# Kernel optimization log

Measured on AMD Instinct MI355X. Metric: run time of the kernel, lower is better.

## Reference

```python
import math
import jax, jax.numpy as jnp
import numpy as np

D = 2048
N = 16
B = 2
L = 4096
SCALE = math.sqrt(1.0 / float(N))


def setup_inputs() -> dict:
    key = jax.random.key(0)
    ks = jax.random.split(key, 6)
    x = jax.random.normal(ks[0], (B, D, L), dtype=jnp.float32)
    alpha = 0.2 * jax.random.normal(ks[1], (D, N, 1), dtype=jnp.float32)
    delta = 0.2 * jax.random.normal(ks[2], (D, N, 1), dtype=jnp.float32)
    theta = 0.2 * jax.random.normal(ks[3], (D, 1, 1), dtype=jnp.float32)
    gamma = jax.random.normal(ks[4], (D, N, 2), dtype=jnp.float32)
    omega = jax.random.normal(ks[5], (D,), dtype=jnp.float32)
    return {"x": x, "alpha": alpha, "delta": delta, "theta": theta,
            "gamma": gamma, "omega": omega}


def _coeffs(alpha, delta, theta, gamma):
    p = jax.nn.sigmoid(alpha)                       # (D, N, 1)
    d = jax.nn.sigmoid(delta)                       # (D, N, 1)
    wave = jnp.arange(1, N + 1, dtype=jnp.float32).reshape(1, N, 1)
    base = jax.nn.sigmoid(theta) * (2.0 * math.pi / float(N))  # (D,1,1)
    phi = wave * base                               # (D, N, 1)
    q = (1.0 - p * d).astype(jnp.complex64) * jnp.exp(1j * phi)  # (D, N, 1)
    gam = (gamma[..., 0] + 1j * gamma[..., 1]) * SCALE            # (D, N)
    return p, q, gam


def _fftconv_real(x, k):
    # x: (B, D, L), k: (D, L)  -> causal conv, keep first L samples
    n = L + L - 1
    n_fft = 1 << (n - 1).bit_length()
    X = jnp.fft.rfft(x, n=n_fft)                    # (B, D, n_fft//2+1)
    K = jnp.fft.rfft(k, n=n_fft)[None]              # (1, D, n_fft//2+1)
    y = jnp.fft.irfft(X * K, n=n_fft)[..., :L]
    return y.astype(x.dtype)


def reference(x, alpha, delta, theta, gamma, omega):
    p, q, gam = _coeffs(alpha, delta, theta, gamma)
    # kernel_d[t] = Re( sum_n p_dn * gamma_dn * q_dn^t )
    t = jnp.arange(L, dtype=jnp.float32)
    V = jnp.exp(t[None, None, :] * jnp.log(q))      # (D, N, L) = q^t
    kernel = jnp.real(jnp.sum(p * gam[..., None] * V, axis=1))  # (D, L)
    y = _fftconv_real(x, kernel) + x * omega[None, :, None]
    # last state: h_t = q * h_{t-1} + p * x_t  (hx = None)
    qs = q[..., 0]                                   # (D, N)
    ps = p[..., 0]                                   # (D, N)
    xs = jnp.moveaxis(x, -1, 0)                      # (L, B, D)
    h0 = jnp.zeros((B, D, N), dtype=jnp.complex64)

    def step(h, xt):
        # xt: (B, D); px_t = p_dn * x_t[b,d]
        h = qs[None] * h + ps[None] * xt[..., None].astype(jnp.complex64)
        return h, None

    h_last, _ = jax.lax.scan(step, h0, xs)
    h_ri = jnp.stack([h_last.real, h_last.imag], axis=-1)  # (B, D, N, 2)
    return y, h_ri
```

## Files before the change

kernel.cpp:

```cpp
#include <hip/hip_runtime.h>
#include <math.h>


constexpr int kD = 2048, kN = 16, kB = 2, kL = 4096;
constexpr int kT   = 128;
constexpr int kCH  = kL / kT;
constexpr int kRPB = 4;
constexpr int kGrid = (kB * kD) / kRPB;
constexpr float kSCALE = 0.25f;

__global__ __launch_bounds__(kT, 2) void fused_kernel(
    const float* __restrict__ x,     const float* __restrict__ alpha,
    const float* __restrict__ delta, const float* __restrict__ theta,
    const float* __restrict__ gamma, const float* __restrict__ omega,
    float* __restrict__ y,           float* __restrict__ hout)
{
    __shared__ float c2a[2][kN], ccc[2][kN], caa[2][kN], cbb[2][kN];
    __shared__ float cc1[2][kN], cc2[2][kN], cpr[2][kN];
    __shared__ float pubs[2][kN], pubp[2][kN];

    const int tid   = threadIdx.x;
    const int llane = tid & 63;
    const bool w1   = (tid >= 64);
    const int row0  = blockIdx.x * kRPB;

    float4 tb[8];
    {
        const float4* xp = (const float4*)(x + (size_t)row0 * kL + (size_t)tid * kCH);
#pragma unroll
        for (int k = 0; k < 8; k++) tb[k] = xp[k];
    }

#pragma unroll 1
    for (int r = 0; r < kRPB; ++r) {
        const int row = row0 + r;
        const int d   = row & (kD - 1);
        const int pp  = r & 1;

        if (tid < kN) {
            int n = tid, i = d * kN + n;
            float p  = 1.0f / (1.0f + expf(-alpha[i]));
            float dd = 1.0f / (1.0f + expf(-delta[i]));
            float th = 1.0f / (1.0f + expf(-theta[d]));
            float phi = (float)(n + 1) * th * 0.39269908169872414f;
            float rr = 1.0f - p * dd;
            float sn, cs;
            sincosf(phi, &sn, &cs);
            float a = rr * cs, b = rr * sn;
            float gr = p * kSCALE * gamma[2 * i];
            float gi = -(p * kSCALE * gamma[2 * i + 1]);
            c2a[pp][n] = a + a;
            ccc[pp][n] = __builtin_fmaf(a, a, b * b);
            caa[pp][n] = a;
            cbb[pp][n] = b;
            cc1[pp][n] = gr;
            cc2[pp][n] = __builtin_fmaf(gi, b, -(gr * a));
            cpr[pp][n] = p;
        }

        float xs[kCH];
#pragma unroll
        for (int k = 0; k < 8; k++) {
            xs[4*k+0] = tb[k].x; xs[4*k+1] = tb[k].y;
            xs[4*k+2] = tb[k].z; xs[4*k+3] = tb[k].w;
        }
        __syncthreads();

        float twoa[kN], cc[kN];
#pragma unroll
        for (int n = 0; n < kN; n++) { twoa[n] = c2a[pp][n]; cc[n] = ccc[pp][n]; }

        float ss[kN], sq[kN];
#pragma unroll
        for (int n = 0; n < kN; n++) { ss[n] = xs[0]; sq[n] = 0.0f; }
#pragma unroll
        for (int j = 1; j < kCH; j++) {
            float xj = xs[j];
#pragma unroll
            for (int n = 0; n < kN; n++) {
                float t  = __builtin_fmaf(-cc[n], sq[n], xj);
                float sn = __builtin_fmaf(twoa[n], ss[n], t);
                sq[n] = ss[n];
                ss[n] = sn;
            }
        }

        float al[kN], be[kN];
        {
            float aa[kN];
#pragma unroll
            for (int n = 0; n < kN; n++) {
                aa[n] = caa[pp][n];
                al[n] = twoa[n];
                be[n] = 1.0f;
            }
#pragma unroll
            for (int sdb = 0; sdb < 4; sdb++) {
#pragma unroll
                for (int n = 0; n < kN; n++) {
                    float t  = __builtin_fmaf(-cc[n], be[n], aa[n] * al[n]);
                    float nb = __builtin_fmaf(-cc[n], be[n] * be[n], al[n] * al[n]);
                    al[n] = (al[n] + al[n]) * t;
                    be[n] = nb;
                }
            }
        }

        float Wa[kN], Wb[kN];
#pragma unroll
        for (int n = 0; n < kN; n++) { Wa[n] = al[n]; Wb[n] = be[n]; }
#pragma unroll
        for (int rd = 0; rd < 6; rd++) {
            const int sh = 1 << rd;
#pragma unroll
            for (int n = 0; n < kN; n++) {
                float cb  = cc[n] * be[n];
                float e00 = __builtin_fmaf(twoa[n], al[n], -cb);
                float e01 = -(cc[n] * al[n]);
                float ts  = __shfl_up(ss[n], (unsigned)sh, 64);
                float tp  = __shfl_up(sq[n], (unsigned)sh, 64);
                if (llane >= sh) {
                    ss[n] = __builtin_fmaf(e00, ts,
                            __builtin_fmaf(e01, tp, ss[n]));
                    sq[n] = __builtin_fmaf(al[n], ts,
                            __builtin_fmaf(-cb, tp, sq[n]));
                }
            }
            if (w1 && (llane & sh)) {
#pragma unroll
                for (int n = 0; n < kN; n++) {
                    float t1 = Wa[n] * al[n];
                    float t2 = Wb[n] * be[n];
                    float t3 = __builtin_fmaf(Wa[n], be[n], al[n] * Wb[n]);
                    Wa[n] = __builtin_fmaf(twoa[n], t1, -(cc[n] * t3));
                    Wb[n] = __builtin_fmaf(-cc[n], t2, t1);
                }
            }
            if (rd < 5) {
#pragma unroll
                for (int n = 0; n < kN; n++) {
                    float t  = __builtin_fmaf(-cc[n], be[n],
                               0.5f * (twoa[n] * al[n]));
                    float nb = __builtin_fmaf(-cc[n], be[n] * be[n],
                                              al[n] * al[n]);
                    al[n] = (al[n] + al[n]) * t;
                    be[n] = nb;
                }
            }
        }

        if (tid == 63) {
#pragma unroll
            for (int n = 0; n < kN; n++) { pubs[pp][n] = ss[n]; pubp[pp][n] = sq[n]; }
        }
        __syncthreads();
        if (w1) {
#pragma unroll
            for (int n = 0; n < kN; n++) {
                float cb  = cc[n] * Wb[n];
                float e00 = __builtin_fmaf(twoa[n], Wa[n], -cb);
                float e01 = -(cc[n] * Wa[n]);
                float ps  = pubs[pp][n], pq = pubp[pp][n];
                ss[n] = __builtin_fmaf(e00, ps,
                        __builtin_fmaf(e01, pq, ss[n]));
                sq[n] = __builtin_fmaf(Wa[n], ps,
                        __builtin_fmaf(-cb, pq, sq[n]));
            }
        }

        if (tid == kT - 1) {
            float4* hp = (float4*)(hout + (size_t)row * (kN * 2));
#pragma unroll
            for (int k = 0; k < kN / 2; k++) {
                int n0 = 2 * k, n1 = 2 * k + 1;
                float hr0 = cpr[pp][n0] *
                            __builtin_fmaf(-caa[pp][n0], sq[n0], ss[n0]);
                float hi0 = cpr[pp][n0] * cbb[pp][n0] * sq[n0];
                float hr1 = cpr[pp][n1] *
                            __builtin_fmaf(-caa[pp][n1], sq[n1], ss[n1]);
                float hi1 = cpr[pp][n1] * cbb[pp][n1] * sq[n1];
                hp[k] = make_float4(hr0, hi0, hr1, hi1);
            }
        }

#pragma unroll
        for (int n = 0; n < kN; n++) {
            float ts = __shfl_up(ss[n], 1, 64);
            float tp = __shfl_up(sq[n], 1, 64);
            ss[n] = ts; sq[n] = tp;
        }
        if (llane == 0) {
#pragma unroll
            for (int n = 0; n < kN; n++) {
                ss[n] = (tid == 0) ? 0.0f : pubs[pp][n];
                sq[n] = (tid == 0) ? 0.0f : pubp[pp][n];
            }
        }

        if (r + 1 < kRPB) {
            const float4* xn = (const float4*)(x + (size_t)(row + 1) * kL +
                                               (size_t)tid * kCH);
#pragma unroll
            for (int k = 0; k < 8; k++) tb[k] = xn[k];
        }

        float c1[kN], c2[kN];
#pragma unroll
        for (int n = 0; n < kN; n++) { c1[n] = cc1[pp][n]; c2[n] = cc2[pp][n]; }
        const float om = omega[d];

        float ys[kCH];
#pragma unroll
        for (int j = 0; j < kCH; j++) {
            float xj = xs[j];
            float acc0 = om * xj, acc1 = 0.0f, acc2 = 0.0f, acc3 = 0.0f;
#pragma unroll
            for (int n = 0; n < kN; n += 4) {
                float t, sn;
                t  = __builtin_fmaf(-cc[n],   sq[n],   xj);
                sn = __builtin_fmaf(twoa[n],  ss[n],   t);
                acc0 = __builtin_fmaf(c1[n],   sn,     acc0);
                acc0 = __builtin_fmaf(c2[n],   ss[n],  acc0);
                sq[n] = ss[n]; ss[n] = sn;
                t  = __builtin_fmaf(-cc[n+1], sq[n+1], xj);
                sn = __builtin_fmaf(twoa[n+1], ss[n+1], t);
                acc1 = __builtin_fmaf(c1[n+1], sn,     acc1);
                acc1 = __builtin_fmaf(c2[n+1], ss[n+1], acc1);
                sq[n+1] = ss[n+1]; ss[n+1] = sn;
                t  = __builtin_fmaf(-cc[n+2], sq[n+2], xj);
                sn = __builtin_fmaf(twoa[n+2], ss[n+2], t);
                acc2 = __builtin_fmaf(c1[n+2], sn,     acc2);
                acc2 = __builtin_fmaf(c2[n+2], ss[n+2], acc2);
                sq[n+2] = ss[n+2]; ss[n+2] = sn;
                t  = __builtin_fmaf(-cc[n+3], sq[n+3], xj);
                sn = __builtin_fmaf(twoa[n+3], ss[n+3], t);
                acc3 = __builtin_fmaf(c1[n+3], sn,     acc3);
                acc3 = __builtin_fmaf(c2[n+3], ss[n+3], acc3);
                sq[n+3] = ss[n+3]; ss[n+3] = sn;
            }
            ys[j] = (acc0 + acc1) + (acc2 + acc3);
        }

        float4* yp = (float4*)(y + (size_t)row * kL + (size_t)tid * kCH);
#pragma unroll
        for (int k = 0; k < 8; k++)
            yp[k] = make_float4(ys[4*k+0], ys[4*k+1], ys[4*k+2], ys[4*k+3]);
    }
}

extern "C" void kernel_launch(void* const* d_in, const int* in_sizes, int n_in,
                              void* d_out, int out_size, void* d_ws, size_t ws_size,
                              hipStream_t stream) {
    const float* x     = (const float*)d_in[0];
    const float* alpha = (const float*)d_in[1];
    const float* delta = (const float*)d_in[2];
    const float* theta = (const float*)d_in[3];
    const float* gamma = (const float*)d_in[4];
    const float* omega = (const float*)d_in[5];
    float* y    = (float*)d_out;
    float* hout = y + (size_t)kB * kD * kL;

    fused_kernel<<<kGrid, kT, 0, stream>>>(x, alpha, delta, theta, gamma,
                                           omega, y, hout);
}
```

Measured before the change: 193.4 us.

## Process one row per block instead of looping over four rows

Drops the per-block loop over four (batch, channel) rows with prefetching of the next row's input. The kernel now launches one block per row (4096 blocks) and relaxes launch bounds from 2 to 1 blocks per SM, which gives the compiler more registers. It also reuses the xs array for outputs instead of a separate ys array to cut register pressure. In exchange it loses the overlap of the next row's loads with the current row's compute and pays per-block setup more often.

```diff
diff --git a/kernel.cpp b/kernel.cpp
--- a/kernel.cpp
+++ b/kernel.cpp
@@ -3,249 +3,217 @@
 
 
 constexpr int kD = 2048, kN = 16, kB = 2, kL = 4096;
-constexpr int kT   = 128;
-constexpr int kCH  = kL / kT;
-constexpr int kRPB = 4;
-constexpr int kGrid = (kB * kD) / kRPB;
+constexpr int kT  = 128;
+constexpr int kCH = kL / kT;
 constexpr float kSCALE = 0.25f;
 
-__global__ __launch_bounds__(kT, 2) void fused_kernel(
+__global__ __launch_bounds__(kT, 1) void fused_kernel(
     const float* __restrict__ x,     const float* __restrict__ alpha,
     const float* __restrict__ delta, const float* __restrict__ theta,
     const float* __restrict__ gamma, const float* __restrict__ omega,
     float* __restrict__ y,           float* __restrict__ hout)
 {
-    __shared__ float c2a[2][kN], ccc[2][kN], caa[2][kN], cbb[2][kN];
-    __shared__ float cc1[2][kN], cc2[2][kN], cpr[2][kN];
-    __shared__ float pubs[2][kN], pubp[2][kN];
-
+    __shared__ float c2a[kN], ccc[kN], caa[kN], cbb[kN];
+    __shared__ float cc1[kN], cc2[kN], cpr[kN];
+    __shared__ float pubs[kN], pubp[kN];
+
+    const int row   = blockIdx.x;
+    const int d     = row & (kD - 1);
     const int tid   = threadIdx.x;
     const int llane = tid & 63;
     const bool w1   = (tid >= 64);
-    const int row0  = blockIdx.x * kRPB;
-
-    float4 tb[8];
+
+    float xs[kCH];
     {
-        const float4* xp = (const float4*)(x + (size_t)row0 * kL + (size_t)tid * kCH);
+        const float4* xp = (const float4*)(x + (size_t)row * kL + (size_t)tid * kCH);
+        float4 tb[8];
 #pragma unroll
         for (int k = 0; k < 8; k++) tb[k] = xp[k];
-    }
-
-#pragma unroll 1
-    for (int r = 0; r < kRPB; ++r) {
-        const int row = row0 + r;
-        const int d   = row & (kD - 1);
-        const int pp  = r & 1;
-
-        if (tid < kN) {
-            int n = tid, i = d * kN + n;
-            float p  = 1.0f / (1.0f + expf(-alpha[i]));
-            float dd = 1.0f / (1.0f + expf(-delta[i]));
-            float th = 1.0f / (1.0f + expf(-theta[d]));
-            float phi = (float)(n + 1) * th * 0.39269908169872414f;
-            float rr = 1.0f - p * dd;
-            float sn, cs;
-            sincosf(phi, &sn, &cs);
-            float a = rr * cs, b = rr * sn;
-            float gr = p * kSCALE * gamma[2 * i];
-            float gi = -(p * kSCALE * gamma[2 * i + 1]);
-            c2a[pp][n] = a + a;
-            ccc[pp][n] = __builtin_fmaf(a, a, b * b);
-            caa[pp][n] = a;
-            cbb[pp][n] = b;
-            cc1[pp][n] = gr;
-            cc2[pp][n] = __builtin_fmaf(gi, b, -(gr * a));
-            cpr[pp][n] = p;
-        }
-
-        float xs[kCH];
 #pragma unroll
         for (int k = 0; k < 8; k++) {
             xs[4*k+0] = tb[k].x; xs[4*k+1] = tb[k].y;
             xs[4*k+2] = tb[k].z; xs[4*k+3] = tb[k].w;
         }
-        __syncthreads();
-
-        float twoa[kN], cc[kN];
-#pragma unroll
-        for (int n = 0; n < kN; n++) { twoa[n] = c2a[pp][n]; cc[n] = ccc[pp][n]; }
-
-        float ss[kN], sq[kN];
-#pragma unroll
-        for (int n = 0; n < kN; n++) { ss[n] = xs[0]; sq[n] = 0.0f; }
-#pragma unroll
-        for (int j = 1; j < kCH; j++) {
-            float xj = xs[j];
+    }
+
+    if (tid < kN) {
+        int n = tid, i = d * kN + n;
+        float p  = 1.0f / (1.0f + expf(-alpha[i]));
+        float dd = 1.0f / (1.0f + expf(-delta[i]));
+        float th = 1.0f / (1.0f + expf(-theta[d]));
+        float phi = (float)(n + 1) * th * 0.39269908169872414f;
+        float rr = 1.0f - p * dd;
+        float sn, cs;
+        sincosf(phi, &sn, &cs);
+        float a = rr * cs, b = rr * sn;
+        float gr = p * kSCALE * gamma[2 * i];
+        float gi = -(p * kSCALE * gamma[2 * i + 1]);
+        c2a[n] = a + a;
+        ccc[n] = __builtin_fmaf(a, a, b * b);
+        caa[n] = a;
+        cbb[n] = b;
+        cc1[n] = gr;
+        cc2[n] = __builtin_fmaf(gi, b, -(gr * a));
+        cpr[n] = p;
+    }
+    __syncthreads();
+
+    float twoa[kN], cc[kN];
+#pragma unroll
+    for (int n = 0; n < kN; n++) { twoa[n] = c2a[n]; cc[n] = ccc[n]; }
+
+    float ss[kN], sq[kN];
+#pragma unroll
+    for (int n = 0; n < kN; n++) { ss[n] = xs[0]; sq[n] = 0.0f; }
+#pragma unroll
+    for (int j = 1; j < kCH; j++) {
+        float xj = xs[j];
+#pragma unroll
+        for (int n = 0; n < kN; n++) {
+            float t  = __builtin_fmaf(-cc[n], sq[n], xj);
+            float sn = __builtin_fmaf(twoa[n], ss[n], t);
+            sq[n] = ss[n];
+            ss[n] = sn;
+        }
+    }
+
+    float al[kN], be[kN];
+#pragma unroll
+    for (int n = 0; n < kN; n++) { al[n] = twoa[n]; be[n] = 1.0f; }
+#pragma unroll
+    for (int sdb = 0; sdb < 4; sdb++) {
+#pragma unroll
+        for (int n = 0; n < kN; n++) {
+            float t  = __builtin_fmaf(-cc[n], be[n], 0.5f * (twoa[n] * al[n]));
+            float nb = __builtin_fmaf(-cc[n], be[n] * be[n], al[n] * al[n]);
+            al[n] = (al[n] + al[n]) * t;
+            be[n] = nb;
+        }
+    }
+
+    float Wa[kN], Wb[kN];
+#pragma unroll
+    for (int n = 0; n < kN; n++) { Wa[n] = al[n]; Wb[n] = be[n]; }
+#pragma unroll
+    for (int rd = 0; rd < 6; rd++) {
+        const int sh = 1 << rd;
+#pragma unroll
+        for (int n = 0; n < kN; n++) {
+            float cb  = cc[n] * be[n];
+            float e00 = __builtin_fmaf(twoa[n], al[n], -cb);
+            float e01 = -(cc[n] * al[n]);
+            float ts  = __shfl_up(ss[n], (unsigned)sh, 64);
+            float tp  = __shfl_up(sq[n], (unsigned)sh, 64);
+            if (llane >= sh) {
+                ss[n] = __builtin_fmaf(e00, ts, __builtin_fmaf(e01, tp, ss[n]));
+                sq[n] = __builtin_fmaf(al[n], ts, __builtin_fmaf(-cb, tp, sq[n]));
+            }
+        }
+        if (w1 && (llane & sh)) {
 #pragma unroll
             for (int n = 0; n < kN; n++) {
-                float t  = __builtin_fmaf(-cc[n], sq[n], xj);
-                float sn = __builtin_fmaf(twoa[n], ss[n], t);
-                sq[n] = ss[n];
-                ss[n] = sn;
+                float t1 = Wa[n] * al[n];
+                float t2 = Wb[n] * be[n];
+                float t3 = __builtin_fmaf(Wa[n], be[n], al[n] * Wb[n]);
+                Wa[n] = __builtin_fmaf(twoa[n], t1, -(cc[n] * t3));
+                Wb[n] = __builtin_fmaf(-cc[n], t2, t1);
             }
         }
-
-        float al[kN], be[kN];
-        {
-            float aa[kN];
+        if (rd < 5) {
 #pragma unroll
             for (int n = 0; n < kN; n++) {
-                aa[n] = caa[pp][n];
-                al[n] = twoa[n];
-                be[n] = 1.0f;
+                float t  = __builtin_fmaf(-cc[n], be[n], 0.5f * (twoa[n] * al[n]));
+                float nb = __builtin_fmaf(-cc[n], be[n] * be[n], al[n] * al[n]);
+                al[n] = (al[n] + al[n]) * t;
+                be[n] = nb;
             }
-#pragma unroll
-            for (int sdb = 0; sdb < 4; sdb++) {
-#pragma unroll
-                for (int n = 0; n < kN; n++) {
-                    float t  = __builtin_fmaf(-cc[n], be[n], aa[n] * al[n]);
-                    float nb = __builtin_fmaf(-cc[n], be[n] * be[n], al[n] * al[n]);
-                    al[n] = (al[n] + al[n]) * t;
-                    be[n] = nb;
-                }
-            }
-        }
-
-        float Wa[kN], Wb[kN];
-#pragma unroll
-        for (int n = 0; n < kN; n++) { Wa[n] = al[n]; Wb[n] = be[n]; }
-#pragma unroll
-        for (int rd = 0; rd < 6; rd++) {
-            const int sh = 1 << rd;
-#pragma unroll
-            for (int n = 0; n < kN; n++) {
-                float cb  = cc[n] * be[n];
-                float e00 = __builtin_fmaf(twoa[n], al[n], -cb);
-                float e01 = -(cc[n] * al[n]);
-                float ts  = __shfl_up(ss[n], (unsigned)sh, 64);
-                float tp  = __shfl_up(sq[n], (unsigned)sh, 64);
-                if (llane >= sh) {
-                    ss[n] = __builtin_fmaf(e00, ts,
-                            __builtin_fmaf(e01, tp, ss[n]));
-                    sq[n] = __builtin_fmaf(al[n], ts,
-                            __builtin_fmaf(-cb, tp, sq[n]));
-                }
-            }
-            if (w1 && (llane & sh)) {
-#pragma unroll
-                for (int n = 0; n < kN; n++) {
-                    float t1 = Wa[n] * al[n];
-                    float t2 = Wb[n] * be[n];
-                    float t3 = __builtin_fmaf(Wa[n], be[n], al[n] * Wb[n]);
-                    Wa[n] = __builtin_fmaf(twoa[n], t1, -(cc[n] * t3));
-                    Wb[n] = __builtin_fmaf(-cc[n], t2, t1);
-                }
-            }
-            if (rd < 5) {
-#pragma unroll
-                for (int n = 0; n < kN; n++) {
-                    float t  = __builtin_fmaf(-cc[n], be[n],
-                               0.5f * (twoa[n] * al[n]));
-                    float nb = __builtin_fmaf(-cc[n], be[n] * be[n],
-                                              al[n] * al[n]);
-                    al[n] = (al[n] + al[n]) * t;
-                    be[n] = nb;
-                }
-            }
-        }
-
-        if (tid == 63) {
-#pragma unroll
-            for (int n = 0; n < kN; n++) { pubs[pp][n] = ss[n]; pubp[pp][n] = sq[n]; }
-        }
-        __syncthreads();
-        if (w1) {
-#pragma unroll
-            for (int n = 0; n < kN; n++) {
-                float cb  = cc[n] * Wb[n];
-                float e00 = __builtin_fmaf(twoa[n], Wa[n], -cb);
-                float e01 = -(cc[n] * Wa[n]);
-                float ps  = pubs[pp][n], pq = pubp[pp][n];
-                ss[n] = __builtin_fmaf(e00, ps,
-                        __builtin_fmaf(e01, pq, ss[n]));
-                sq[n] = __builtin_fmaf(Wa[n], ps,
-                        __builtin_fmaf(-cb, pq, sq[n]));
-            }
-        }
-
-        if (tid == kT - 1) {
-            float4* hp = (float4*)(hout + (size_t)row * (kN * 2));
-#pragma unroll
-            for (int k = 0; k < kN / 2; k++) {
-                int n0 = 2 * k, n1 = 2 * k + 1;
-                float hr0 = cpr[pp][n0] *
-                            __builtin_fmaf(-caa[pp][n0], sq[n0], ss[n0]);
-                float hi0 = cpr[pp][n0] * cbb[pp][n0] * sq[n0];
-                float hr1 = cpr[pp][n1] *
-                            __builtin_fmaf(-caa[pp][n1], sq[n1], ss[n1]);
-                float hi1 = cpr[pp][n1] * cbb[pp][n1] * sq[n1];
-                hp[k] = make_float4(hr0, hi0, hr1, hi1);
-            }
-        }
-
-#pragma unroll
-        for (int n = 0; n < kN; n++) {
-            float ts = __shfl_up(ss[n], 1, 64);
-            float tp = __shfl_up(sq[n], 1, 64);
-            ss[n] = ts; sq[n] = tp;
-        }
-        if (llane == 0) {
-#pragma unroll
-            for (int n = 0; n < kN; n++) {
-                ss[n] = (tid == 0) ? 0.0f : pubs[pp][n];
-                sq[n] = (tid == 0) ? 0.0f : pubp[pp][n];
-            }
-        }
-
-        if (r + 1 < kRPB) {
-            const float4* xn = (const float4*)(x + (size_t)(row + 1) * kL +
-                                               (size_t)tid * kCH);
-#pragma unroll
-            for (int k = 0; k < 8; k++) tb[k] = xn[k];
-        }
-
-        float c1[kN], c2[kN];
-#pragma unroll
-        for (int n = 0; n < kN; n++) { c1[n] = cc1[pp][n]; c2[n] = cc2[pp][n]; }
-        const float om = omega[d];
-
-        float ys[kCH];
-#pragma unroll
-        for (int j = 0; j < kCH; j++) {
-            float xj = xs[j];
-            float acc0 = om * xj, acc1 = 0.0f, acc2 = 0.0f, acc3 = 0.0f;
-#pragma unroll
-            for (int n = 0; n < kN; n += 4) {
-                float t, sn;
-                t  = __builtin_fmaf(-cc[n],   sq[n],   xj);
-                sn = __builtin_fmaf(twoa[n],  ss[n],   t);
-                acc0 = __builtin_fmaf(c1[n],   sn,     acc0);
-                acc0 = __builtin_fmaf(c2[n],   ss[n],  acc0);
-                sq[n] = ss[n]; ss[n] = sn;
-                t  = __builtin_fmaf(-cc[n+1], sq[n+1], xj);
-                sn = __builtin_fmaf(twoa[n+1], ss[n+1], t);
-                acc1 = __builtin_fmaf(c1[n+1], sn,     acc1);
-                acc1 = __builtin_fmaf(c2[n+1], ss[n+1], acc1);
-                sq[n+1] = ss[n+1]; ss[n+1] = sn;
-                t  = __builtin_fmaf(-cc[n+2], sq[n+2], xj);
-                sn = __builtin_fmaf(twoa[n+2], ss[n+2], t);
-                acc2 = __builtin_fmaf(c1[n+2], sn,     acc2);
-                acc2 = __builtin_fmaf(c2[n+2], ss[n+2], acc2);
-                sq[n+2] = ss[n+2]; ss[n+2] = sn;
-                t  = __builtin_fmaf(-cc[n+3], sq[n+3], xj);
-                sn = __builtin_fmaf(twoa[n+3], ss[n+3], t);
-                acc3 = __builtin_fmaf(c1[n+3], sn,     acc3);
-                acc3 = __builtin_fmaf(c2[n+3], ss[n+3], acc3);
-                sq[n+3] = ss[n+3]; ss[n+3] = sn;
-            }
-            ys[j] = (acc0 + acc1) + (acc2 + acc3);
-        }
-
-        float4* yp = (float4*)(y + (size_t)row * kL + (size_t)tid * kCH);
-#pragma unroll
-        for (int k = 0; k < 8; k++)
-            yp[k] = make_float4(ys[4*k+0], ys[4*k+1], ys[4*k+2], ys[4*k+3]);
-    }
+        }
+    }
+
+    if (tid == 63) {
+#pragma unroll
+        for (int n = 0; n < kN; n++) { pubs[n] = ss[n]; pubp[n] = sq[n]; }
+    }
+    __syncthreads();
+    if (w1) {
+#pragma unroll
+        for (int n = 0; n < kN; n++) {
+            float cb  = cc[n] * Wb[n];
+            float e00 = __builtin_fmaf(twoa[n], Wa[n], -cb);
+            float e01 = -(cc[n] * Wa[n]);
+            float ps  = pubs[n], pq = pubp[n];
+            ss[n] = __builtin_fmaf(e00, ps, __builtin_fmaf(e01, pq, ss[n]));
+            sq[n] = __builtin_fmaf(Wa[n], ps, __builtin_fmaf(-cb, pq, sq[n]));
+        }
+    }
+
+    if (tid == kT - 1) {
+        float4* hp = (float4*)(hout + (size_t)row * (kN * 2));
+#pragma unroll
+        for (int k = 0; k < kN / 2; k++) {
+            int n0 = 2 * k, n1 = 2 * k + 1;
+            float hr0 = cpr[n0] * __builtin_fmaf(-caa[n0], sq[n0], ss[n0]);
+            float hi0 = cpr[n0] * cbb[n0] * sq[n0];
+            float hr1 = cpr[n1] * __builtin_fmaf(-caa[n1], sq[n1], ss[n1]);
+            float hi1 = cpr[n1] * cbb[n1] * sq[n1];
+            hp[k] = make_float4(hr0, hi0, hr1, hi1);
+        }
+    }
+
+#pragma unroll
+    for (int n = 0; n < kN; n++) {
+        float ts = __shfl_up(ss[n], 1, 64);
+        float tp = __shfl_up(sq[n], 1, 64);
+        ss[n] = ts; sq[n] = tp;
+    }
+    if (llane == 0) {
+#pragma unroll
+        for (int n = 0; n < kN; n++) {
+            ss[n] = (tid == 0) ? 0.0f : pubs[n];
+            sq[n] = (tid == 0) ? 0.0f : pubp[n];
+        }
+    }
+
+    float c1[kN], c2[kN];
+#pragma unroll
+    for (int n = 0; n < kN; n++) { c1[n] = cc1[n]; c2[n] = cc2[n]; }
+    const float om = omega[d];
+
+#pragma unroll
+    for (int j = 0; j < kCH; j++) {
+        float xj = xs[j];
+        float acc0 = om * xj, acc1 = 0.0f, acc2 = 0.0f, acc3 = 0.0f;
+#pragma unroll
+        for (int n = 0; n < kN; n += 4) {
+            float t, sn;
+            t  = __builtin_fmaf(-cc[n],    sq[n],    xj);
+            sn = __builtin_fmaf(twoa[n],   ss[n],    t);
+            acc0 = __builtin_fmaf(c1[n],   sn,       acc0);
+            acc0 = __builtin_fmaf(c2[n],   ss[n],    acc0);
+            sq[n] = ss[n]; ss[n] = sn;
+            t  = __builtin_fmaf(-cc[n+1],  sq[n+1],  xj);
+            sn = __builtin_fmaf(twoa[n+1], ss[n+1],  t);
+            acc1 = __builtin_fmaf(c1[n+1], sn,       acc1);
+            acc1 = __builtin_fmaf(c2[n+1], ss[n+1],  acc1);
+            sq[n+1] = ss[n+1]; ss[n+1] = sn;
+            t  = __builtin_fmaf(-cc[n+2],  sq[n+2],  xj);
+            sn = __builtin_fmaf(twoa[n+2], ss[n+2],  t);
+            acc2 = __builtin_fmaf(c1[n+2], sn,       acc2);
+            acc2 = __builtin_fmaf(c2[n+2], ss[n+2],  acc2);
+            sq[n+2] = ss[n+2]; ss[n+2] = sn;
+            t  = __builtin_fmaf(-cc[n+3],  sq[n+3],  xj);
+            sn = __builtin_fmaf(twoa[n+3], ss[n+3],  t);
+            acc3 = __builtin_fmaf(c1[n+3], sn,       acc3);
+            acc3 = __builtin_fmaf(c2[n+3], ss[n+3],  acc3);
+            sq[n+3] = ss[n+3]; ss[n+3] = sn;
+        }
+        xs[j] = (acc0 + acc1) + (acc2 + acc3);
+    }
+
+    float4* yp = (float4*)(y + (size_t)row * kL + (size_t)tid * kCH);
+#pragma unroll
+    for (int k = 0; k < 8; k++)
+        yp[k] = make_float4(xs[4*k+0], xs[4*k+1], xs[4*k+2], xs[4*k+3]);
 }
 
 extern "C" void kernel_launch(void* const* d_in, const int* in_sizes, int n_in,
@@ -260,6 +228,6 @@
     float* y    = (float*)d_out;
     float* hout = y + (size_t)kB * kD * kL;
 
-    fused_kernel<<<kGrid, kT, 0, stream>>>(x, alpha, delta, theta, gamma,
-                                           omega, y, hout);
+    fused_kernel<<<kB * kD, kT, 0, stream>>>(x, alpha, delta, theta, gamma,
+                                             omega, y, hout);
 }
```

New measurement: 179.6 us. 1.08x faster.
